# Optimization experiments

Measured on AMD Instinct MI355X. Metric: run time of the kernel, lower is better.

The kernel has to match this reference:

```python
import jax, jax.numpy as jnp
import numpy as np
import math

B, N, C = 8, 2048, 512

def setup_inputs() -> dict:
    key = jax.random.key(0)
    ks = jax.random.split(key, 7)
    s = 1.0 / math.sqrt(C)
    return {
        "feature": jax.random.normal(ks[0], (B, N, C), dtype=jnp.float32),
        "wq": jax.random.uniform(ks[1], (C, C), jnp.float32, -s, s),
        "bq": jax.random.uniform(ks[2], (C,), jnp.float32, -s, s),
        "wk": jax.random.uniform(ks[3], (C, C), jnp.float32, -s, s),
        "bk": jax.random.uniform(ks[4], (C,), jnp.float32, -s, s),
        "wv": jax.random.uniform(ks[5], (C, C), jnp.float32, -s, s),
        "bv": jax.random.uniform(ks[6], (C,), jnp.float32, -s, s),
    }

def reference(feature, wq, bq, wk, bk, wv, bv):
    # torch nn.Linear: x @ W.T + b
    q = jnp.einsum('bnc,dc->bnd', feature, wq) + bq
    k = jnp.einsum('bnc,dc->bnd', feature, wk) + bk
    v = jnp.einsum('bnc,dc->bnd', feature, wv) + bv
    scores = jnp.einsum('bnd,bmd->bnm', q, k)          # [B, N, N]
    attn = jax.nn.softmax(scores, axis=2) / math.sqrt(C)  # post-softmax scale (as in source)
    v_star = jnp.einsum('bnm,bmd->bnd', attn, v)
    return feature + v_star
```

## Files before the change

kernel.cpp:

```cpp
#include <hip/hip_runtime.h>
#include <cstdint>
#include <cstddef>


typedef __bf16 bf16x8 __attribute__((ext_vector_type(8)));
typedef float f32x4 __attribute__((ext_vector_type(4)));
typedef short short4v __attribute__((ext_vector_type(4)));
typedef short short8v __attribute__((ext_vector_type(8)));

__device__ __forceinline__ float b2f(short s) {
  union { float f; unsigned u; } u; u.u = ((unsigned)(unsigned short)s) << 16; return u.f;
}
__device__ __forceinline__ short f2b(float f) {
  union { float f; unsigned u; } u; u.f = f;
  unsigned r = (u.u + 0x7fffu + ((u.u >> 16) & 1u)) >> 16;
  return (short)r;
}

#define GLDS(gptr, lptr) \
  __builtin_amdgcn_global_load_lds( \
      (const __attribute__((address_space(1))) unsigned int*)(const void*)(gptr), \
      (__attribute__((address_space(3))) unsigned int*)(void*)(lptr), 16, 0, 0)

__global__ __launch_bounds__(256) void prep(const float* __restrict__ f,
                                            const float* __restrict__ w0,
                                            const float* __restrict__ w1,
                                            const float* __restrict__ w2,
                                            const float* __restrict__ b0,
                                            const float* __restrict__ b1,
                                            const float* __restrict__ b2,
                                            short* __restrict__ Xb, short* __restrict__ Wb,
                                            float* __restrict__ biasP, float* __restrict__ l) {
  const int bid = blockIdx.x;
  const int t = threadIdx.x;
  if (bid < 8192) {
    int i = bid * 256 + t;
    float4 v = ((const float4*)f)[i];
    short4v o = { f2b(v.x), f2b(v.y), f2b(v.z), f2b(v.w) };
    *(short4v*)(Xb + (size_t)i * 4) = o;
  } else if (bid < 8960) {
    int i = (bid - 8192) * 256 + t;
    const float* src = (i < 65536) ? w0 : (i < 131072) ? w1 : w2;
    float4 v = ((const float4*)src)[i & 65535];
    short4v o = { f2b(v.x), f2b(v.y), f2b(v.z), f2b(v.w) };
    *(short4v*)(Wb + (size_t)i * 4) = o;
  } else {
    int i = (bid - 8960) * 256 + t;
    float4 z = { 0.f, 0.f, 0.f, 0.f };
    ((float4*)l)[i * 2] = z;
    ((float4*)l)[i * 2 + 1] = z;
    if (i < 1536) {
      const float* s = (i < 512) ? b0 : (i < 1024) ? b1 : b2;
      biasP[i] = s[i & 511];
    }
  }
}

__global__ __launch_bounds__(256) void gemm_qkv(const short* __restrict__ X,
                                                const short* __restrict__ Wall,
                                                const float* __restrict__ biasP,
                                                short* __restrict__ Out) {
  __shared__ __align__(16) short Xs[128 * 64];
  __shared__ __align__(16) short Ws[128 * 64];
  const int z = blockIdx.z;
  const short* Wm = Wall + (size_t)z * 262144;
  const int m0 = blockIdx.y * 128, n0 = blockIdx.x * 128;
  const int t = threadIdx.x;
  const int lane = t & 63, w = t >> 6;
  const int wn = (w & 1) * 64, wm = (w >> 1) * 64;
  const int fr = lane & 15, l4 = lane >> 4;

  f32x4 acc[4][4] = {};

  for (int k0 = 0; k0 < 512; k0 += 64) {
    __syncthreads();
#pragma unroll
    for (int u = 0; u < 4; ++u) {
      int cc = t + u * 256;
      int r = cc >> 3, cs = cc & 7;
      int kk = ((cs ^ (r & 7)) * 8);
      GLDS(X + (size_t)(m0 + r) * 512 + k0 + kk, Xs + cc * 8);
      GLDS(Wm + (size_t)(n0 + r) * 512 + k0 + kk, Ws + cc * 8);
    }
    __syncthreads();
#pragma unroll
    for (int h = 0; h < 2; ++h) {
      bf16x8 wf[4], xf[4];
#pragma unroll
      for (int i = 0; i < 4; ++i)
        wf[i] = *(const bf16x8*)(Ws + (wn + i * 16 + fr) * 64 + (((h * 4 + l4) ^ (fr & 7)) * 8));
#pragma unroll
      for (int j = 0; j < 4; ++j)
        xf[j] = *(const bf16x8*)(Xs + (wm + j * 16 + fr) * 64 + (((h * 4 + l4) ^ (fr & 7)) * 8));
#pragma unroll
      for (int i = 0; i < 4; ++i)
#pragma unroll
        for (int j = 0; j < 4; ++j)
          acc[i][j] = __builtin_amdgcn_mfma_f32_16x16x32_bf16(wf[i], xf[j], acc[i][j], 0, 0, 0);
    }
  }

  const int rq = l4 * 4;
#pragma unroll
  for (int i = 0; i < 4; ++i) {
    int nb = n0 + wn + i * 16 + rq;
    float4 bs = *(const float4*)(biasP + z * 512 + nb);
#pragma unroll
    for (int j = 0; j < 4; ++j) {
      int m = m0 + wm + j * 16 + fr;
      short4v o = { f2b(acc[i][j][0] + bs.x), f2b(acc[i][j][1] + bs.y),
                    f2b(acc[i][j][2] + bs.z), f2b(acc[i][j][3] + bs.w) };
      *(short4v*)(Out + (size_t)z * 8388608 + (size_t)m * 512 + nb) = o;
    }
  }
}

__global__ __launch_bounds__(256) void gemm_qk(const short* __restrict__ Q,
                                               const short* __restrict__ Kb,
                                               short* __restrict__ P,
                                               float* __restrict__ l) {
  __shared__ __align__(16) short Qs[128 * 64];
  __shared__ __align__(16) short Ks[128 * 64];
  const int z = blockIdx.z;
  const short* A = Q + (size_t)z * 2048 * 512;
  const short* Bm = Kb + (size_t)z * 2048 * 512;
  const int m0 = blockIdx.y * 128, n0 = blockIdx.x * 128;
  const int t = threadIdx.x;
  const int lane = t & 63, w = t >> 6;
  const int wn = (w & 1) * 64, wm = (w >> 1) * 64;
  const int fr = lane & 15, l4 = lane >> 4;

  f32x4 acc[4][4] = {};

  for (int k0 = 0; k0 < 512; k0 += 64) {
    __syncthreads();
#pragma unroll
    for (int u = 0; u < 4; ++u) {
      int cc = t + u * 256;
      int r = cc >> 3, cs = cc & 7;
      int kk = ((cs ^ (r & 7)) * 8);
      GLDS(A + (size_t)(m0 + r) * 512 + k0 + kk, Qs + cc * 8);
      GLDS(Bm + (size_t)(n0 + r) * 512 + k0 + kk, Ks + cc * 8);
    }
    __syncthreads();
#pragma unroll
    for (int h = 0; h < 2; ++h) {
      bf16x8 kf[4], qf[4];
#pragma unroll
      for (int i = 0; i < 4; ++i)
        kf[i] = *(const bf16x8*)(Ks + (wn + i * 16 + fr) * 64 + (((h * 4 + l4) ^ (fr & 7)) * 8));
#pragma unroll
      for (int j = 0; j < 4; ++j)
        qf[j] = *(const bf16x8*)(Qs + (wm + j * 16 + fr) * 64 + (((h * 4 + l4) ^ (fr & 7)) * 8));
#pragma unroll
      for (int i = 0; i < 4; ++i)
#pragma unroll
        for (int j = 0; j < 4; ++j)
          acc[i][j] = __builtin_amdgcn_mfma_f32_16x16x32_bf16(kf[i], qf[j], acc[i][j], 0, 0, 0);
    }
  }

  const int rq = l4 * 4;
  float rs[4] = { 0.f, 0.f, 0.f, 0.f };
#pragma unroll
  for (int i = 0; i < 4; ++i) {
    int nb = n0 + wn + i * 16 + rq;
#pragma unroll
    for (int j = 0; j < 4; ++j) {
      int m = m0 + wm + j * 16 + fr;
      short4v o;
      float part = 0.f;
#pragma unroll
      for (int r = 0; r < 4; ++r) {
        float e = exp2f(acc[i][j][r] * 1.4426950408889634f);
        short eb = f2b(e);
        o[r] = eb;
        part += b2f(eb);
      }
      *(short4v*)(P + (size_t)z * 4194304 + (size_t)m * 2048 + nb) = o;
      rs[j] += part;
    }
  }
#pragma unroll
  for (int j = 0; j < 4; ++j) {
    rs[j] += __shfl_xor(rs[j], 16);
    rs[j] += __shfl_xor(rs[j], 32);
  }
  if (lane < 16) {
#pragma unroll
    for (int j = 0; j < 4; ++j)
      atomicAdd(&l[z * 2048 + m0 + wm + j * 16 + fr], rs[j]);
  }
}

__global__ __launch_bounds__(256) void gemm_pv(const short* __restrict__ Pm,
                                               const short* __restrict__ Vt,
                                               const float* __restrict__ l,
                                               const float* __restrict__ resid,
                                               float* __restrict__ out, float scale) {
  __shared__ __align__(16) short Ps[64 * 64];
  __shared__ __align__(16) short Vs[128 * 64];
  const int z = blockIdx.z;
  const short* A = Pm + (size_t)z * 4194304;
  const short* Bm = Vt + (size_t)z * 1048576;
  const int m0 = blockIdx.y * 64, n0 = blockIdx.x * 128;
  const int t = threadIdx.x;
  const int lane = t & 63, w = t >> 6;
  const int wn = (w & 1) * 64, wm = (w >> 1) * 32;
  const int fr = lane & 15, l4 = lane >> 4;

  f32x4 acc[4][2] = {};

  for (int k0 = 0; k0 < 2048; k0 += 64) {
    __syncthreads();
#pragma unroll
    for (int u = 0; u < 2; ++u) {
      int cc = t + u * 256;
      int r = cc >> 3, cs = cc & 7;
      int kk = ((cs ^ (r & 7)) * 8);
      GLDS(A + (size_t)(m0 + r) * 2048 + k0 + kk, Ps + cc * 8);
    }
#pragma unroll
    for (int u = 0; u < 4; ++u) {
      int cc = t + u * 256;
      int r = cc >> 3, cs = cc & 7;
      int kk = ((cs ^ (r & 7)) * 8);
      GLDS(Bm + (size_t)(n0 + r) * 2048 + k0 + kk, Vs + cc * 8);
    }
    __syncthreads();
#pragma unroll
    for (int h = 0; h < 2; ++h) {
      bf16x8 vf[4], pf[2];
#pragma unroll
      for (int i = 0; i < 4; ++i)
        vf[i] = *(const bf16x8*)(Vs + (wn + i * 16 + fr) * 64 + (((h * 4 + l4) ^ (fr & 7)) * 8));
#pragma unroll
      for (int j = 0; j < 2; ++j)
        pf[j] = *(const bf16x8*)(Ps + (wm + j * 16 + fr) * 64 + (((h * 4 + l4) ^ (fr & 7)) * 8));
#pragma unroll
      for (int i = 0; i < 4; ++i)
#pragma unroll
        for (int j = 0; j < 2; ++j)
          acc[i][j] = __builtin_amdgcn_mfma_f32_16x16x32_bf16(vf[i], pf[j], acc[i][j], 0, 0, 0);
    }
  }

  const int rq = l4 * 4;
#pragma unroll
  for (int j = 0; j < 2; ++j) {
    int m = m0 + wm + j * 16 + fr;
    float linv = scale / l[z * 2048 + m];
#pragma unroll
    for (int i = 0; i < 4; ++i) {
      int nb = n0 + wn + i * 16 + rq;
      size_t idx = (size_t)z * 1048576 + (size_t)m * 512 + nb;
      float4 rv = *(const float4*)(resid + idx);
      float4 o = { rv.x + acc[i][j][0] * linv, rv.y + acc[i][j][1] * linv,
                   rv.z + acc[i][j][2] * linv, rv.w + acc[i][j][3] * linv };
      *(float4*)(out + idx) = o;
    }
  }
}

__global__ __launch_bounds__(256) void transpose64(const short* __restrict__ V,
                                                   short* __restrict__ Vt) {
  __shared__ short tile[64][72];
  const int b = blockIdx.z;
  const int d0 = blockIdx.x * 64, n0 = blockIdx.y * 64;
  const int t = threadIdx.x;
#pragma unroll
  for (int h = 0; h < 2; ++h) {
    int c = t + h * 256;
    int r = c >> 3, cj = (c & 7) * 8;
    short8v val = *(const short8v*)(V + ((size_t)(b * 2048 + n0 + r)) * 512 + d0 + cj);
#pragma unroll
    for (int j = 0; j < 8; ++j) tile[r][cj + j] = val[j];
  }
  __syncthreads();
#pragma unroll
  for (int h = 0; h < 2; ++h) {
    int c = t + h * 256;
    int dr = c >> 3, nj = (c & 7) * 8;
    short8v o;
#pragma unroll
    for (int j = 0; j < 8; ++j) o[j] = tile[nj + j][dr];
    *(short8v*)(Vt + ((size_t)b * 512 + d0 + dr) * 2048 + n0 + nj) = o;
  }
}

extern "C" void kernel_launch(void* const* d_in, const int* in_sizes, int n_in,
                              void* d_out, int out_size, void* d_ws, size_t ws_size,
                              hipStream_t stream) {
  const float* feature = (const float*)d_in[0];
  const float* wq = (const float*)d_in[1];
  const float* bq = (const float*)d_in[2];
  const float* wk = (const float*)d_in[3];
  const float* bk = (const float*)d_in[4];
  const float* wv = (const float*)d_in[5];
  const float* bv = (const float*)d_in[6];
  float* out = (float*)d_out;

  const size_t MN = (size_t)16384 * 512;
  short* Xb = (short*)d_ws;
  short* Wb = Xb + MN;
  short* Q = Wb + 786432;
  short* K = Q + MN;
  short* V = K + MN;
  short* Vt = V + MN;
  short* P = Vt + MN;
  float* biasP = (float*)(P + (size_t)8 * 2048 * 2048);
  float* l = biasP + 1536;

  prep<<<8968, 256, 0, stream>>>(feature, wq, wk, wv, bq, bk, bv, Xb, Wb, biasP, l);

  gemm_qkv<<<dim3(4, 128, 3), 256, 0, stream>>>(Xb, Wb, biasP, Q);
  transpose64<<<dim3(8, 32, 8), 256, 0, stream>>>(V, Vt);
  gemm_qk<<<dim3(16, 16, 8), 256, 0, stream>>>(Q, K, P, l);

  const float iscl = 0.044194173824159216f;
  gemm_pv<<<dim3(4, 32, 8), 256, 0, stream>>>(P, Vt, l, feature, out, iscl);
}
```

Baseline: 266.8 us.

## Fuse V transpose into QKV GEMM epilogue and enlarge QK/PV work per block

The V projection now swaps the MFMA operand order so its epilogue writes V already transposed, which removes the separate transpose kernel and one round trip of V through memory. gemm_qk has each block loop over four N tiles, cutting row-sum atomics by a factor of four, and sums the fp32 exp values rather than the bf16-rounded ones. gemm_pv now computes two 128-wide V tiles per block, so each P tile is loaded once for both and P traffic is halved. The cost is fewer blocks (less parallelism) for the QK and PV launches and more registers and LDS per block in PV.

```diff
diff --git a/kernel.cpp b/kernel.cpp
--- a/kernel.cpp
+++ b/kernel.cpp
@@ -59,7 +59,8 @@
 __global__ __launch_bounds__(256) void gemm_qkv(const short* __restrict__ X,
                                                 const short* __restrict__ Wall,
                                                 const float* __restrict__ biasP,
-                                                short* __restrict__ Out) {
+                                                short* __restrict__ Out,
+                                                short* __restrict__ VtOut) {
   __shared__ __align__(16) short Xs[128 * 64];
   __shared__ __align__(16) short Ws[128 * 64];
   const int z = blockIdx.z;
@@ -92,25 +93,50 @@
 #pragma unroll
       for (int j = 0; j < 4; ++j)
         xf[j] = *(const bf16x8*)(Xs + (wm + j * 16 + fr) * 64 + (((h * 4 + l4) ^ (fr & 7)) * 8));
-#pragma unroll
-      for (int i = 0; i < 4; ++i)
-#pragma unroll
-        for (int j = 0; j < 4; ++j)
-          acc[i][j] = __builtin_amdgcn_mfma_f32_16x16x32_bf16(wf[i], xf[j], acc[i][j], 0, 0, 0);
+      if (z < 2) {
+#pragma unroll
+        for (int i = 0; i < 4; ++i)
+#pragma unroll
+          for (int j = 0; j < 4; ++j)
+            acc[i][j] = __builtin_amdgcn_mfma_f32_16x16x32_bf16(wf[i], xf[j], acc[i][j], 0, 0, 0);
+      } else {
+#pragma unroll
+        for (int i = 0; i < 4; ++i)
+#pragma unroll
+          for (int j = 0; j < 4; ++j)
+            acc[i][j] = __builtin_amdgcn_mfma_f32_16x16x32_bf16(xf[i], wf[j], acc[i][j], 0, 0, 0);
+      }
     }
   }
 
   const int rq = l4 * 4;
-#pragma unroll
-  for (int i = 0; i < 4; ++i) {
-    int nb = n0 + wn + i * 16 + rq;
-    float4 bs = *(const float4*)(biasP + z * 512 + nb);
+  if (z < 2) {
+#pragma unroll
+    for (int i = 0; i < 4; ++i) {
+      int nb = n0 + wn + i * 16 + rq;
+      float4 bs = *(const float4*)(biasP + z * 512 + nb);
+#pragma unroll
+      for (int j = 0; j < 4; ++j) {
+        int m = m0 + wm + j * 16 + fr;
+        short4v o = { f2b(acc[i][j][0] + bs.x), f2b(acc[i][j][1] + bs.y),
+                      f2b(acc[i][j][2] + bs.z), f2b(acc[i][j][3] + bs.w) };
+        *(short4v*)(Out + (size_t)z * 8388608 + (size_t)m * 512 + nb) = o;
+      }
+    }
+  } else {
+    const int zB = blockIdx.y >> 4;
+    const int mb = (m0 & 2047);
 #pragma unroll
     for (int j = 0; j < 4; ++j) {
-      int m = m0 + wm + j * 16 + fr;
-      short4v o = { f2b(acc[i][j][0] + bs.x), f2b(acc[i][j][1] + bs.y),
-                    f2b(acc[i][j][2] + bs.z), f2b(acc[i][j][3] + bs.w) };
-      *(short4v*)(Out + (size_t)z * 8388608 + (size_t)m * 512 + nb) = o;
+      int d = n0 + wn + j * 16 + fr;
+      float bd = biasP[1024 + d];
+#pragma unroll
+      for (int i = 0; i < 4; ++i) {
+        int mloc = mb + wm + i * 16 + rq;
+        short4v o = { f2b(acc[i][j][0] + bd), f2b(acc[i][j][1] + bd),
+                      f2b(acc[i][j][2] + bd), f2b(acc[i][j][3] + bd) };
+        *(short4v*)(VtOut + (size_t)zB * 1048576 + (size_t)d * 2048 + mloc) = o;
+      }
     }
   }
 }
@@ -124,63 +150,68 @@
   const int z = blockIdx.z;
   const short* A = Q + (size_t)z * 2048 * 512;
   const short* Bm = Kb + (size_t)z * 2048 * 512;
-  const int m0 = blockIdx.y * 128, n0 = blockIdx.x * 128;
+  const int m0 = blockIdx.y * 128;
+  const int n_base = blockIdx.x * 512;
   const int t = threadIdx.x;
   const int lane = t & 63, w = t >> 6;
   const int wn = (w & 1) * 64, wm = (w >> 1) * 64;
   const int fr = lane & 15, l4 = lane >> 4;
-
-  f32x4 acc[4][4] = {};
-
-  for (int k0 = 0; k0 < 512; k0 += 64) {
-    __syncthreads();
-#pragma unroll
-    for (int u = 0; u < 4; ++u) {
-      int cc = t + u * 256;
-      int r = cc >> 3, cs = cc & 7;
-      int kk = ((cs ^ (r & 7)) * 8);
-      GLDS(A + (size_t)(m0 + r) * 512 + k0 + kk, Qs + cc * 8);
-      GLDS(Bm + (size_t)(n0 + r) * 512 + k0 + kk, Ks + cc * 8);
-    }
-    __syncthreads();
-#pragma unroll
-    for (int h = 0; h < 2; ++h) {
-      bf16x8 kf[4], qf[4];
-#pragma unroll
-      for (int i = 0; i < 4; ++i)
-        kf[i] = *(const bf16x8*)(Ks + (wn + i * 16 + fr) * 64 + (((h * 4 + l4) ^ (fr & 7)) * 8));
-#pragma unroll
-      for (int j = 0; j < 4; ++j)
-        qf[j] = *(const bf16x8*)(Qs + (wm + j * 16 + fr) * 64 + (((h * 4 + l4) ^ (fr & 7)) * 8));
-#pragma unroll
-      for (int i = 0; i < 4; ++i)
+  const int rq = l4 * 4;
+
+  float rs[4] = { 0.f, 0.f, 0.f, 0.f };
+
+  for (int nt = 0; nt < 4; ++nt) {
+    const int n0 = n_base + nt * 128;
+    f32x4 acc[4][4] = {};
+
+    for (int k0 = 0; k0 < 512; k0 += 64) {
+      __syncthreads();
+#pragma unroll
+      for (int u = 0; u < 4; ++u) {
+        int cc = t + u * 256;
+        int r = cc >> 3, cs = cc & 7;
+        int kk = ((cs ^ (r & 7)) * 8);
+        GLDS(A + (size_t)(m0 + r) * 512 + k0 + kk, Qs + cc * 8);
+        GLDS(Bm + (size_t)(n0 + r) * 512 + k0 + kk, Ks + cc * 8);
+      }
+      __syncthreads();
+#pragma unroll
+      for (int h = 0; h < 2; ++h) {
+        bf16x8 kf[4], qf[4];
+#pragma unroll
+        for (int i = 0; i < 4; ++i)
+          kf[i] = *(const bf16x8*)(Ks + (wn + i * 16 + fr) * 64 + (((h * 4 + l4) ^ (fr & 7)) * 8));
 #pragma unroll
         for (int j = 0; j < 4; ++j)
-          acc[i][j] = __builtin_amdgcn_mfma_f32_16x16x32_bf16(kf[i], qf[j], acc[i][j], 0, 0, 0);
-    }
-  }
-
-  const int rq = l4 * 4;
-  float rs[4] = { 0.f, 0.f, 0.f, 0.f };
-#pragma unroll
-  for (int i = 0; i < 4; ++i) {
-    int nb = n0 + wn + i * 16 + rq;
-#pragma unroll
-    for (int j = 0; j < 4; ++j) {
-      int m = m0 + wm + j * 16 + fr;
-      short4v o;
-      float part = 0.f;
-#pragma unroll
-      for (int r = 0; r < 4; ++r) {
-        float e = exp2f(acc[i][j][r] * 1.4426950408889634f);
-        short eb = f2b(e);
-        o[r] = eb;
-        part += b2f(eb);
-      }
-      *(short4v*)(P + (size_t)z * 4194304 + (size_t)m * 2048 + nb) = o;
-      rs[j] += part;
-    }
-  }
+          qf[j] = *(const bf16x8*)(Qs + (wm + j * 16 + fr) * 64 + (((h * 4 + l4) ^ (fr & 7)) * 8));
+#pragma unroll
+        for (int i = 0; i < 4; ++i)
+#pragma unroll
+          for (int j = 0; j < 4; ++j)
+            acc[i][j] = __builtin_amdgcn_mfma_f32_16x16x32_bf16(kf[i], qf[j], acc[i][j], 0, 0, 0);
+      }
+    }
+
+#pragma unroll
+    for (int i = 0; i < 4; ++i) {
+      int nb = n0 + wn + i * 16 + rq;
+#pragma unroll
+      for (int j = 0; j < 4; ++j) {
+        int m = m0 + wm + j * 16 + fr;
+        short4v o;
+        float part = 0.f;
+#pragma unroll
+        for (int r = 0; r < 4; ++r) {
+          float e = exp2f(acc[i][j][r] * 1.4426950408889634f);
+          o[r] = f2b(e);
+          part += e;
+        }
+        *(short4v*)(P + (size_t)z * 4194304 + (size_t)m * 2048 + nb) = o;
+        rs[j] += part;
+      }
+    }
+  }
+
 #pragma unroll
   for (int j = 0; j < 4; ++j) {
     rs[j] += __shfl_xor(rs[j], 16);
@@ -199,17 +230,17 @@
                                                const float* __restrict__ resid,
                                                float* __restrict__ out, float scale) {
   __shared__ __align__(16) short Ps[64 * 64];
-  __shared__ __align__(16) short Vs[128 * 64];
+  __shared__ __align__(16) short Vs[2][128 * 64];
   const int z = blockIdx.z;
   const short* A = Pm + (size_t)z * 4194304;
   const short* Bm = Vt + (size_t)z * 1048576;
-  const int m0 = blockIdx.y * 64, n0 = blockIdx.x * 128;
+  const int m0 = blockIdx.y * 64, n0 = blockIdx.x * 256;
   const int t = threadIdx.x;
   const int lane = t & 63, w = t >> 6;
   const int wn = (w & 1) * 64, wm = (w >> 1) * 32;
   const int fr = lane & 15, l4 = lane >> 4;
 
-  f32x4 acc[4][2] = {};
+  f32x4 acc[2][4][2] = {};
 
   for (int k0 = 0; k0 < 2048; k0 += 64) {
     __syncthreads();
@@ -221,27 +252,33 @@
       GLDS(A + (size_t)(m0 + r) * 2048 + k0 + kk, Ps + cc * 8);
     }
 #pragma unroll
-    for (int u = 0; u < 4; ++u) {
-      int cc = t + u * 256;
-      int r = cc >> 3, cs = cc & 7;
-      int kk = ((cs ^ (r & 7)) * 8);
-      GLDS(Bm + (size_t)(n0 + r) * 2048 + k0 + kk, Vs + cc * 8);
-    }
+    for (int nt = 0; nt < 2; ++nt)
+#pragma unroll
+      for (int u = 0; u < 4; ++u) {
+        int cc = t + u * 256;
+        int r = cc >> 3, cs = cc & 7;
+        int kk = ((cs ^ (r & 7)) * 8);
+        GLDS(Bm + (size_t)(n0 + nt * 128 + r) * 2048 + k0 + kk, Vs[nt] + cc * 8);
+      }
     __syncthreads();
 #pragma unroll
     for (int h = 0; h < 2; ++h) {
-      bf16x8 vf[4], pf[2];
-#pragma unroll
-      for (int i = 0; i < 4; ++i)
-        vf[i] = *(const bf16x8*)(Vs + (wn + i * 16 + fr) * 64 + (((h * 4 + l4) ^ (fr & 7)) * 8));
+      bf16x8 pf[2];
 #pragma unroll
       for (int j = 0; j < 2; ++j)
         pf[j] = *(const bf16x8*)(Ps + (wm + j * 16 + fr) * 64 + (((h * 4 + l4) ^ (fr & 7)) * 8));
 #pragma unroll
-      for (int i = 0; i < 4; ++i)
-#pragma unroll
-        for (int j = 0; j < 2; ++j)
-          acc[i][j] = __builtin_amdgcn_mfma_f32_16x16x32_bf16(vf[i], pf[j], acc[i][j], 0, 0, 0);
+      for (int nt = 0; nt < 2; ++nt) {
+        bf16x8 vf[4];
+#pragma unroll
+        for (int i = 0; i < 4; ++i)
+          vf[i] = *(const bf16x8*)(Vs[nt] + (wn + i * 16 + fr) * 64 + (((h * 4 + l4) ^ (fr & 7)) * 8));
+#pragma unroll
+        for (int i = 0; i < 4; ++i)
+#pragma unroll
+          for (int j = 0; j < 2; ++j)
+            acc[nt][i][j] = __builtin_amdgcn_mfma_f32_16x16x32_bf16(vf[i], pf[j], acc[nt][i][j], 0, 0, 0);
+      }
     }
   }
 
@@ -251,40 +288,16 @@
     int m = m0 + wm + j * 16 + fr;
     float linv = scale / l[z * 2048 + m];
 #pragma unroll
-    for (int i = 0; i < 4; ++i) {
-      int nb = n0 + wn + i * 16 + rq;
-      size_t idx = (size_t)z * 1048576 + (size_t)m * 512 + nb;
-      float4 rv = *(const float4*)(resid + idx);
-      float4 o = { rv.x + acc[i][j][0] * linv, rv.y + acc[i][j][1] * linv,
-                   rv.z + acc[i][j][2] * linv, rv.w + acc[i][j][3] * linv };
-      *(float4*)(out + idx) = o;
-    }
-  }
-}
-
-__global__ __launch_bounds__(256) void transpose64(const short* __restrict__ V,
-                                                   short* __restrict__ Vt) {
-  __shared__ short tile[64][72];
-  const int b = blockIdx.z;
-  const int d0 = blockIdx.x * 64, n0 = blockIdx.y * 64;
-  const int t = threadIdx.x;
-#pragma unroll
-  for (int h = 0; h < 2; ++h) {
-    int c = t + h * 256;
-    int r = c >> 3, cj = (c & 7) * 8;
-    short8v val = *(const short8v*)(V + ((size_t)(b * 2048 + n0 + r)) * 512 + d0 + cj);
-#pragma unroll
-    for (int j = 0; j < 8; ++j) tile[r][cj + j] = val[j];
-  }
-  __syncthreads();
-#pragma unroll
-  for (int h = 0; h < 2; ++h) {
-    int c = t + h * 256;
-    int dr = c >> 3, nj = (c & 7) * 8;
-    short8v o;
-#pragma unroll
-    for (int j = 0; j < 8; ++j) o[j] = tile[nj + j][dr];
-    *(short8v*)(Vt + ((size_t)b * 512 + d0 + dr) * 2048 + n0 + nj) = o;
+    for (int nt = 0; nt < 2; ++nt)
+#pragma unroll
+      for (int i = 0; i < 4; ++i) {
+        int nb = n0 + nt * 128 + wn + i * 16 + rq;
+        size_t idx = (size_t)z * 1048576 + (size_t)m * 512 + nb;
+        float4 rv = *(const float4*)(resid + idx);
+        float4 o = { rv.x + acc[nt][i][j][0] * linv, rv.y + acc[nt][i][j][1] * linv,
+                     rv.z + acc[nt][i][j][2] * linv, rv.w + acc[nt][i][j][3] * linv };
+        *(float4*)(out + idx) = o;
+      }
   }
 }
 
@@ -305,18 +318,16 @@
   short* Wb = Xb + MN;
   short* Q = Wb + 786432;
   short* K = Q + MN;
-  short* V = K + MN;
-  short* Vt = V + MN;
+  short* Vt = K + MN;
   short* P = Vt + MN;
   float* biasP = (float*)(P + (size_t)8 * 2048 * 2048);
   float* l = biasP + 1536;
 
   prep<<<8968, 256, 0, stream>>>(feature, wq, wk, wv, bq, bk, bv, Xb, Wb, biasP, l);
 
-  gemm_qkv<<<dim3(4, 128, 3), 256, 0, stream>>>(Xb, Wb, biasP, Q);
-  transpose64<<<dim3(8, 32, 8), 256, 0, stream>>>(V, Vt);
-  gemm_qk<<<dim3(16, 16, 8), 256, 0, stream>>>(Q, K, P, l);
+  gemm_qkv<<<dim3(4, 128, 3), 256, 0, stream>>>(Xb, Wb, biasP, Q, Vt);
+  gemm_qk<<<dim3(4, 16, 8), 256, 0, stream>>>(Q, K, P, l);
 
   const float iscl = 0.044194173824159216f;
-  gemm_pv<<<dim3(4, 32, 8), 256, 0, stream>>>(P, Vt, l, feature, out, iscl);
-}
+  gemm_pv<<<dim3(2, 32, 8), 256, 0, stream>>>(P, Vt, l, feature, out, iscl);
+}
```

Result: faster. 256.9 us (-3.7%).
